# Kernel tuning notes

Measured on AMD Instinct MI355X. Metric: run time of the kernel, lower is better.

## Reference

```python
import jax, jax.numpy as jnp
import numpy as np

D = 512      # feature_bins
DK = 64      # d_k = d_v
H = 8        # n_heads
EPS = 1e-5


def setup_inputs() -> dict:
    key = jax.random.key(0)
    ks = jax.random.split(key, 12)
    B, S = 4, 2048
    s = 1.0 / np.sqrt(D)
    inp = {
        "Q": jax.random.normal(ks[0], (B, S, D), jnp.float32),
        "K": jax.random.normal(ks[1], (B, S, D), jnp.float32),
        "V": jax.random.normal(ks[2], (B, S, D), jnp.float32),
        # nn.Linear params: weight [out, in], bias [out]
        "Wq": jax.random.normal(ks[3], (H * DK, D), jnp.float32) * s,
        "bq": jnp.zeros((H * DK,), jnp.float32),
        "Wk": jax.random.normal(ks[4], (H * DK, D), jnp.float32) * s,
        "bk": jnp.zeros((H * DK,), jnp.float32),
        "Wv": jax.random.normal(ks[5], (H * DK, D), jnp.float32) * s,
        "bv": jnp.zeros((H * DK,), jnp.float32),
        "Wo": jax.random.normal(ks[6], (D, H * DK), jnp.float32) * s,
        "bo": jnp.zeros((D,), jnp.float32),
        "gamma": jnp.ones((D,), jnp.float32),
        "beta": jnp.zeros((D,), jnp.float32),
    }
    return inp


def _layernorm(x, gamma, beta):
    mu = jnp.mean(x, axis=-1, keepdims=True)
    var = jnp.mean(jnp.square(x - mu), axis=-1, keepdims=True)
    return (x - mu) * jax.lax.rsqrt(var + EPS) * gamma + beta


def reference(Q, K, V, Wq, bq, Wk, bk, Wv, bv, Wo, bo, gamma, beta):
    B, S, _ = Q.shape
    residual = Q
    # projections -> [B, H, S, DK]
    q = (Q @ Wq.T + bq).reshape(B, S, H, DK).transpose(0, 2, 1, 3)
    k = (K @ Wk.T + bk).reshape(B, S, H, DK).transpose(0, 2, 1, 3)
    v = (V @ Wv.T + bv).reshape(B, S, H, DK).transpose(0, 2, 1, 3)
    # NOTE: original code has NO 1/sqrt(d_k) scaling
    scores = jnp.einsum("bhqd,bhkd->bhqk", q, k)
    attn = jax.nn.softmax(scores, axis=-1)
    context = jnp.einsum("bhqk,bhkd->bhqd", attn, v)
    context = context.transpose(0, 2, 1, 3).reshape(B, S, H * DK)
    output = context @ Wo.T + bo
    out = _layernorm(output + residual, gamma, beta)
    return (out, attn)
```

## Files before the change

### kernel.cpp

```cpp
#include <hip/hip_runtime.h>

#define NB 4
#define NS 2048
#define ND 512
#define NH 8
#define NDK 64
#define LN_EPS 1e-5f
#define SCLAMP 80.0f

typedef __attribute__((ext_vector_type(8))) short short8;
typedef __attribute__((ext_vector_type(4))) short s16x4;
typedef __attribute__((ext_vector_type(4))) float f32x4;

__device__ inline short f2bf(float x) {
    unsigned u = __builtin_bit_cast(unsigned, x);
    unsigned r = (u + 0x7FFFu + ((u >> 16) & 1u)) >> 16;
    return (short)r;
}
__device__ inline float bf2f(short h) {
    unsigned u = ((unsigned)(unsigned short)h) << 16;
    return __builtin_bit_cast(float, u);
}
__device__ inline unsigned splitT(float x) {
    unsigned u = __builtin_bit_cast(unsigned, x);
    unsigned h = u >> 16;
    float r = x - bf2f((short)h);
    unsigned l = __builtin_bit_cast(unsigned, r) >> 16;
    return (h & 0xFFFFu) | (l << 16);
}

__device__ inline int swzS(int row, int b8) {
    return row * 64 + (((b8) * 8) ^ ((row & 7) << 3));
}
__device__ inline int swz4(int row, int g4) {
    return row * 64 + ((((g4 >> 1)) * 8) ^ ((row & 7) << 3)) + (g4 & 1) * 4;
}

__global__ __launch_bounds__(256) void k_projm_all(
    const float* __restrict__ Qx, const float* __restrict__ Kx,
    const float* __restrict__ Vx,
    const float* __restrict__ Wq, const float* __restrict__ bq,
    const float* __restrict__ Wk, const float* __restrict__ bk,
    const float* __restrict__ Wv, const float* __restrict__ bv,
    short* __restrict__ qh, short* __restrict__ ql,
    short* __restrict__ kh, short* __restrict__ kl,
    short* __restrict__ vtb)
{
    __shared__ short WsH[8192], WsL[8192];
    const int which = blockIdx.z;
    const float* X    = which == 0 ? Qx : (which == 1 ? Kx : Vx);
    const float* W    = which == 0 ? Wq : (which == 1 ? Wk : Wv);
    const float* bias = which == 0 ? bq : (which == 1 ? bk : bv);
    short* outh       = which == 0 ? qh : (which == 1 ? kh : vtb);
    short* outl       = which == 0 ? ql : kl;

    const int tid = threadIdx.x;
    const int w = tid >> 6, lane = tid & 63;
    const int lr = lane & 15, lg = lane >> 4;
    const int row0 = blockIdx.y * 64;
    const int col0 = blockIdx.x * 128;
    const int xrow = row0 + w * 16 + lr;

    f32x4 acc[8] = {};

    float4 wb[8], ab[4];
#pragma unroll
    for (int i = 0; i < 8; ++i) {
        int idx = tid + 256 * i, wrow = idx >> 4, g4 = idx & 15;
        wb[i] = *(const float4*)&W[(size_t)(col0 + wrow) * ND + g4 * 4];
    }
#pragma unroll
    for (int ks = 0; ks < 2; ++ks) {
        ab[2*ks+0] = *(const float4*)&X[(size_t)xrow * ND + ks * 32 + lg * 8];
        ab[2*ks+1] = *(const float4*)&X[(size_t)xrow * ND + ks * 32 + lg * 8 + 4];
    }

    for (int kc = 0; kc < 8; ++kc) {
        __syncthreads();
#pragma unroll
        for (int i = 0; i < 8; ++i) {
            int idx = tid + 256 * i, wrow = idx >> 4, g4 = idx & 15;
            s16x4 hv, lv;
            unsigned p0 = splitT(wb[i].x), p1 = splitT(wb[i].y);
            unsigned p2 = splitT(wb[i].z), p3 = splitT(wb[i].w);
            hv[0] = (short)p0; lv[0] = (short)(p0 >> 16);
            hv[1] = (short)p1; lv[1] = (short)(p1 >> 16);
            hv[2] = (short)p2; lv[2] = (short)(p2 >> 16);
            hv[3] = (short)p3; lv[3] = (short)(p3 >> 16);
            int off = swz4(wrow, g4);
            *(s16x4*)&WsH[off] = hv;
            *(s16x4*)&WsL[off] = lv;
        }
        __syncthreads();

        short8 ah[2], al[2];
#pragma unroll
        for (int ks = 0; ks < 2; ++ks) {
#pragma unroll
            for (int j = 0; j < 4; ++j) {
                unsigned p = splitT(ab[2*ks][j]);
                ah[ks][j] = (short)p; al[ks][j] = (short)(p >> 16);
            }
#pragma unroll
            for (int j = 0; j < 4; ++j) {
                unsigned p = splitT(ab[2*ks+1][j]);
                ah[ks][4+j] = (short)p; al[ks][4+j] = (short)(p >> 16);
            }
        }

        if (kc < 7) {
            const int kn = (kc + 1) * 64;
#pragma unroll
            for (int i = 0; i < 8; ++i) {
                int idx = tid + 256 * i, wrow = idx >> 4, g4 = idx & 15;
                wb[i] = *(const float4*)&W[(size_t)(col0 + wrow) * ND + kn + g4 * 4];
            }
#pragma unroll
            for (int ks = 0; ks < 2; ++ks) {
                ab[2*ks+0] = *(const float4*)&X[(size_t)xrow * ND + kn + ks * 32 + lg * 8];
                ab[2*ks+1] = *(const float4*)&X[(size_t)xrow * ND + kn + ks * 32 + lg * 8 + 4];
            }
        }

#pragma unroll
        for (int cs = 0; cs < 8; ++cs)
#pragma unroll
            for (int ks = 0; ks < 2; ++ks) {
                short8 fh = *(const short8*)&WsH[swzS(cs * 16 + lr, ks * 4 + lg)];
                short8 fl = *(const short8*)&WsL[swzS(cs * 16 + lr, ks * 4 + lg)];
                acc[cs] = __builtin_amdgcn_mfma_f32_16x16x32_bf16(ah[ks], fh, acc[cs], 0, 0, 0);
                acc[cs] = __builtin_amdgcn_mfma_f32_16x16x32_bf16(ah[ks], fl, acc[cs], 0, 0, 0);
                acc[cs] = __builtin_amdgcn_mfma_f32_16x16x32_bf16(al[ks], fh, acc[cs], 0, 0, 0);
            }
    }

#pragma unroll
    for (int cs = 0; cs < 8; ++cs) {
        int c = col0 + cs * 16 + lr;
        int h_ = c >> 6, dk = c & (NDK - 1);
        float bv = bias[c];
#pragma unroll
        for (int r = 0; r < 4; ++r) {
            int gr = row0 + w * 16 + lg * 4 + r;
            int b_ = gr >> 11, s_ = gr & (NS - 1);
            float x = acc[cs][r] + bv;
            if (which != 2) {
                size_t idx = (((size_t)b_ * NH + h_) * NS + s_) * NDK + dk;
                short hb = f2bf(x);
                outh[idx] = hb;
                outl[idx] = f2bf(x - bf2f(hb));
            } else {
                size_t idx = (((size_t)b_ * NH + h_) * NDK + dk) * NS + s_;
                outh[idx] = f2bf(x);
            }
        }
    }
}

__device__ inline void att_decode2(int wg, int& bh, int& rt) {
    rt = (wg >> 3) & 15;
    bh = (wg & 7) + ((wg >> 7) << 3);
}

__global__ __launch_bounds__(256) void k_pvl(
    const short* __restrict__ qh, const short* __restrict__ ql,
    const short* __restrict__ kh, const short* __restrict__ kl,
    const short* __restrict__ vtb,
    float* __restrict__ iLrow, short* __restrict__ ctxb)
{
    __shared__ short KsH[4096], KsL[4096], Vs[4096];
    __shared__ short plbf[4][32][72];
    const int tid = threadIdx.x;
    const int w = tid >> 6, lane = tid & 63;
    const int lr = lane & 15, lg = lane >> 4;
    int bh, rt;
    att_decode2(blockIdx.x, bh, rt);
    const int row0 = rt * 128 + w * 16;
    const size_t base = (size_t)bh * NS * NDK;
    const short* vb = vtb + (size_t)bh * NDK * NS;
    const int srow0 = tid >> 3, sb8 = tid & 7;
    const int srow1 = srow0 + 32;

    short8 ah[2][2], al[2][2];
#pragma unroll
    for (int st = 0; st < 2; ++st)
#pragma unroll
        for (int ks = 0; ks < 2; ++ks) {
            size_t idx = base + (size_t)(row0 + st * 64 + lr) * NDK + ks * 32 + lg * 8;
            ah[st][ks] = *(const short8*)&qh[idx];
            al[st][ks] = *(const short8*)&ql[idx];
        }

    float lsum[2][4] = {};
    f32x4 vacc[2][4] = {};

    short8 nh0, nh1, nl0, nl1, nv0, nv1;
    {
        nh0 = *(const short8*)&kh[base + (size_t)(srow0) * NDK + sb8 * 8];
        nh1 = *(const short8*)&kh[base + (size_t)(srow1) * NDK + sb8 * 8];
        nl0 = *(const short8*)&kl[base + (size_t)(srow0) * NDK + sb8 * 8];
        nl1 = *(const short8*)&kl[base + (size_t)(srow1) * NDK + sb8 * 8];
        nv0 = *(const short8*)&vb[(size_t)srow0 * NS + sb8 * 8];
        nv1 = *(const short8*)&vb[(size_t)srow1 * NS + sb8 * 8];
    }

    for (int c = 0; c < 32; ++c) {
        short8 ch0 = nh0, ch1 = nh1, cl0 = nl0, cl1 = nl1, cv0 = nv0, cv1 = nv1;
        __syncthreads();
        *(short8*)&KsH[swzS(srow0, sb8)] = ch0;
        *(short8*)&KsH[swzS(srow1, sb8)] = ch1;
        *(short8*)&KsL[swzS(srow0, sb8)] = cl0;
        *(short8*)&KsL[swzS(srow1, sb8)] = cl1;
        *(short8*)&Vs[swzS(srow0, sb8)] = cv0;
        *(short8*)&Vs[swzS(srow1, sb8)] = cv1;
        __syncthreads();

        if (c < 31) {
            const int coln = (c + 1) * 64;
            nh0 = *(const short8*)&kh[base + (size_t)(coln + srow0) * NDK + sb8 * 8];
            nh1 = *(const short8*)&kh[base + (size_t)(coln + srow1) * NDK + sb8 * 8];
            nl0 = *(const short8*)&kl[base + (size_t)(coln + srow0) * NDK + sb8 * 8];
            nl1 = *(const short8*)&kl[base + (size_t)(coln + srow1) * NDK + sb8 * 8];
            nv0 = *(const short8*)&vb[(size_t)srow0 * NS + coln + sb8 * 8];
            nv1 = *(const short8*)&vb[(size_t)srow1 * NS + coln + sb8 * 8];
        }

        f32x4 sa[2][4] = {};
#pragma unroll
        for (int cs = 0; cs < 4; ++cs)
#pragma unroll
            for (int ks = 0; ks < 2; ++ks) {
                short8 fh = *(const short8*)&KsH[swzS(cs * 16 + lr, ks * 4 + lg)];
                short8 fl = *(const short8*)&KsL[swzS(cs * 16 + lr, ks * 4 + lg)];
#pragma unroll
                for (int st = 0; st < 2; ++st) {
                    sa[st][cs] = __builtin_amdgcn_mfma_f32_16x16x32_bf16(ah[st][ks], fh, sa[st][cs], 0, 0, 0);
                    sa[st][cs] = __builtin_amdgcn_mfma_f32_16x16x32_bf16(ah[st][ks], fl, sa[st][cs], 0, 0, 0);
                    sa[st][cs] = __builtin_amdgcn_mfma_f32_16x16x32_bf16(al[st][ks], fh, sa[st][cs], 0, 0, 0);
                }
            }

#pragma unroll
        for (int st = 0; st < 2; ++st)
#pragma unroll
            for (int cs = 0; cs < 4; ++cs)
#pragma unroll
                for (int r = 0; r < 4; ++r) {
                    float e = __expf(fminf(sa[st][cs][r], SCLAMP));
                    lsum[st][r] += e;
                    plbf[w][st * 16 + lg * 4 + r][cs * 16 + lr] = f2bf(e);
                }

#pragma unroll
        for (int k2 = 0; k2 < 2; ++k2) {
            short8 pa0 = *(const short8*)&plbf[w][lr][k2 * 32 + lg * 8];
            short8 pa1 = *(const short8*)&plbf[w][16 + lr][k2 * 32 + lg * 8];
#pragma unroll
            for (int d = 0; d < 4; ++d) {
                short8 vf = *(const short8*)&Vs[swzS(d * 16 + lr, k2 * 4 + lg)];
                vacc[0][d] = __builtin_amdgcn_mfma_f32_16x16x32_bf16(pa0, vf, vacc[0][d], 0, 0, 0);
                vacc[1][d] = __builtin_amdgcn_mfma_f32_16x16x32_bf16(pa1, vf, vacc[1][d], 0, 0, 0);
            }
        }
    }

#pragma unroll
    for (int st = 0; st < 2; ++st)
#pragma unroll
        for (int r = 0; r < 4; ++r)
#pragma unroll
            for (int off = 1; off < 16; off <<= 1)
                lsum[st][r] += __shfl_xor(lsum[st][r], off);

    float iL[2][4];
#pragma unroll
    for (int st = 0; st < 2; ++st)
#pragma unroll
        for (int r = 0; r < 4; ++r) iL[st][r] = 1.0f / lsum[st][r];
    if (lr == 0) {
#pragma unroll
        for (int st = 0; st < 2; ++st)
#pragma unroll
            for (int r = 0; r < 4; ++r)
                iLrow[(size_t)bh * NS + row0 + st * 64 + lg * 4 + r] = iL[st][r];
    }
    const int b_ = bh >> 3, h_ = bh & 7;
#pragma unroll
    for (int st = 0; st < 2; ++st)
#pragma unroll
        for (int d = 0; d < 4; ++d)
#pragma unroll
            for (int r = 0; r < 4; ++r) {
                int row = row0 + st * 64 + lg * 4 + r;
                ctxb[((size_t)b_ * NS + row) * ND + h_ * NDK + d * 16 + lr] =
                    f2bf(vacc[st][d][r] * iL[st][r]);
            }
}

__global__ __launch_bounds__(256) void k_attn_write(
    const short* __restrict__ qh, const short* __restrict__ ql,
    const short* __restrict__ kh, const short* __restrict__ kl,
    const float* __restrict__ iLrow, float* __restrict__ attn)
{
    __shared__ short KsH[4096], KsL[4096];
    const int tid = threadIdx.x;
    const int w = tid >> 6, lane = tid & 63;
    const int lr = lane & 15, lg = lane >> 4;
    int bh, rt;
    att_decode2(blockIdx.x, bh, rt);
    const int row0 = rt * 128 + w * 16;
    const size_t base = (size_t)bh * NS * NDK;
    float* ab = attn + (size_t)bh * NS * NS;
    const int srow0 = tid >> 3, sb8 = tid & 7;
    const int srow1 = srow0 + 32;

    short8 ah[2][2], al[2][2];
#pragma unroll
    for (int st = 0; st < 2; ++st)
#pragma unroll
        for (int ks = 0; ks < 2; ++ks) {
            size_t idx = base + (size_t)(row0 + st * 64 + lr) * NDK + ks * 32 + lg * 8;
            ah[st][ks] = *(const short8*)&qh[idx];
            al[st][ks] = *(const short8*)&ql[idx];
        }
    float iLr[2][4];
#pragma unroll
    for (int st = 0; st < 2; ++st)
#pragma unroll
        for (int r = 0; r < 4; ++r)
            iLr[st][r] = iLrow[(size_t)bh * NS + row0 + st * 64 + lg * 4 + r];

    short8 nh0, nh1, nl0, nl1;
    {
        nh0 = *(const short8*)&kh[base + (size_t)(srow0) * NDK + sb8 * 8];
        nh1 = *(const short8*)&kh[base + (size_t)(srow1) * NDK + sb8 * 8];
        nl0 = *(const short8*)&kl[base + (size_t)(srow0) * NDK + sb8 * 8];
        nl1 = *(const short8*)&kl[base + (size_t)(srow1) * NDK + sb8 * 8];
    }

    for (int c = 0; c < 32; ++c) {
        short8 ch0 = nh0, ch1 = nh1, cl0 = nl0, cl1 = nl1;
        __syncthreads();
        *(short8*)&KsH[swzS(srow0, sb8)] = ch0;
        *(short8*)&KsH[swzS(srow1, sb8)] = ch1;
        *(short8*)&KsL[swzS(srow0, sb8)] = cl0;
        *(short8*)&KsL[swzS(srow1, sb8)] = cl1;
        __syncthreads();

        if (c < 31) {
            const int coln = (c + 1) * 64;
            nh0 = *(const short8*)&kh[base + (size_t)(coln + srow0) * NDK + sb8 * 8];
            nh1 = *(const short8*)&kh[base + (size_t)(coln + srow1) * NDK + sb8 * 8];
            nl0 = *(const short8*)&kl[base + (size_t)(coln + srow0) * NDK + sb8 * 8];
            nl1 = *(const short8*)&kl[base + (size_t)(coln + srow1) * NDK + sb8 * 8];
        }

        const int col0 = c * 64;
        f32x4 sa[2][4] = {};
#pragma unroll
        for (int cs = 0; cs < 4; ++cs)
#pragma unroll
            for (int ks = 0; ks < 2; ++ks) {
                short8 fh = *(const short8*)&KsH[swzS(cs * 16 + lr, ks * 4 + lg)];
                short8 fl = *(const short8*)&KsL[swzS(cs * 16 + lr, ks * 4 + lg)];
#pragma unroll
                for (int st = 0; st < 2; ++st) {
                    sa[st][cs] = __builtin_amdgcn_mfma_f32_16x16x32_bf16(ah[st][ks], fh, sa[st][cs], 0, 0, 0);
                    sa[st][cs] = __builtin_amdgcn_mfma_f32_16x16x32_bf16(ah[st][ks], fl, sa[st][cs], 0, 0, 0);
                    sa[st][cs] = __builtin_amdgcn_mfma_f32_16x16x32_bf16(al[st][ks], fh, sa[st][cs], 0, 0, 0);
                }
            }

#pragma unroll
        for (int st = 0; st < 2; ++st)
#pragma unroll
            for (int cs = 0; cs < 4; ++cs)
#pragma unroll
                for (int r = 0; r < 4; ++r) {
                    float p = __expf(fminf(sa[st][cs][r], SCLAMP)) * iLr[st][r];
                    ab[(size_t)(row0 + st * 64 + lg * 4 + r) * NS + col0 + cs * 16 + lr] = p;
                }
    }
}

__global__ __launch_bounds__(256) void k_outproj_m(
    const short* __restrict__ Xc, const float* __restrict__ W,
    const float* __restrict__ bias, const float* __restrict__ Qin,
    float* __restrict__ out)
{
    __shared__ short WsH[8192], WsL[8192];
    const int tid = threadIdx.x;
    const int w = tid >> 6, lane = tid & 63;
    const int lr = lane & 15, lg = lane >> 4;
    const int row0 = blockIdx.y * 64;
    const int col0 = blockIdx.x * 128;
    const int xrow = row0 + w * 16 + lr;

    f32x4 acc[8] = {};

    float4 wb[8];
    short8 abn[2];
#pragma unroll
    for (int i = 0; i < 8; ++i) {
        int idx = tid + 256 * i, wrow = idx >> 4, g4 = idx & 15;
        wb[i] = *(const float4*)&W[(size_t)(col0 + wrow) * ND + g4 * 4];
    }
#pragma unroll
    for (int ks = 0; ks < 2; ++ks)
        abn[ks] = *(const short8*)&Xc[(size_t)xrow * ND + ks * 32 + lg * 8];

    for (int kc = 0; kc < 8; ++kc) {
        __syncthreads();
#pragma unroll
        for (int i = 0; i < 8; ++i) {
            int idx = tid + 256 * i, wrow = idx >> 4, g4 = idx & 15;
            s16x4 hv, lv;
            unsigned p0 = splitT(wb[i].x), p1 = splitT(wb[i].y);
            unsigned p2 = splitT(wb[i].z), p3 = splitT(wb[i].w);
            hv[0] = (short)p0; lv[0] = (short)(p0 >> 16);
            hv[1] = (short)p1; lv[1] = (short)(p1 >> 16);
            hv[2] = (short)p2; lv[2] = (short)(p2 >> 16);
            hv[3] = (short)p3; lv[3] = (short)(p3 >> 16);
            int off = swz4(wrow, g4);
            *(s16x4*)&WsH[off] = hv;
            *(s16x4*)&WsL[off] = lv;
        }
        __syncthreads();

        short8 ah[2] = { abn[0], abn[1] };

        if (kc < 7) {
            const int kn = (kc + 1) * 64;
#pragma unroll
            for (int i = 0; i < 8; ++i) {
                int idx = tid + 256 * i, wrow = idx >> 4, g4 = idx & 15;
                wb[i] = *(const float4*)&W[(size_t)(col0 + wrow) * ND + kn + g4 * 4];
            }
#pragma unroll
            for (int ks = 0; ks < 2; ++ks)
                abn[ks] = *(const short8*)&Xc[(size_t)xrow * ND + kn + ks * 32 + lg * 8];
        }

#pragma unroll
        for (int cs = 0; cs < 8; ++cs)
#pragma unroll
            for (int ks = 0; ks < 2; ++ks) {
                short8 fh = *(const short8*)&WsH[swzS(cs * 16 + lr, ks * 4 + lg)];
                short8 fl = *(const short8*)&WsL[swzS(cs * 16 + lr, ks * 4 + lg)];
                acc[cs] = __builtin_amdgcn_mfma_f32_16x16x32_bf16(ah[ks], fh, acc[cs], 0, 0, 0);
                acc[cs] = __builtin_amdgcn_mfma_f32_16x16x32_bf16(ah[ks], fl, acc[cs], 0, 0, 0);
            }
    }

#pragma unroll
    for (int cs = 0; cs < 8; ++cs) {
        int c = col0 + cs * 16 + lr;
        float bv = bias[c];
#pragma unroll
        for (int r = 0; r < 4; ++r) {
            int gr = row0 + w * 16 + lg * 4 + r;
            float res = Qin[(size_t)gr * ND + c];
            out[(size_t)gr * ND + c] = acc[cs][r] + bv + res;
        }
    }
}

__global__ __launch_bounds__(256) void k_ln(
    float* __restrict__ out, const float* __restrict__ gamma,
    const float* __restrict__ beta)
{
    const int tid = threadIdx.x;
    float* p = out + (size_t)blockIdx.x * ND;
    float2 v = *(const float2*)&p[tid * 2];

    float s = v.x + v.y;
#pragma unroll
    for (int off = 32; off > 0; off >>= 1) s += __shfl_xor(s, off);
    __shared__ float red1[4];
    __shared__ float red2[4];
    if ((tid & 63) == 0) red1[tid >> 6] = s;
    __syncthreads();
    const float mu = (red1[0] + red1[1] + red1[2] + red1[3]) * (1.0f / ND);

    float dx = v.x - mu, dy = v.y - mu;
    float q = dx * dx + dy * dy;
#pragma unroll
    for (int off = 32; off > 0; off >>= 1) q += __shfl_xor(q, off);
    if ((tid & 63) == 0) red2[tid >> 6] = q;
    __syncthreads();
    const float var = (red2[0] + red2[1] + red2[2] + red2[3]) * (1.0f / ND);
    const float inv = rsqrtf(var + LN_EPS);

    float2 g = *(const float2*)&gamma[tid * 2];
    float2 be = *(const float2*)&beta[tid * 2];
    float2 o = { dx * inv * g.x + be.x, dy * inv * g.y + be.y };
    *(float2*)&p[tid * 2] = o;
}

extern "C" void kernel_launch(void* const* d_in, const int* in_sizes, int n_in,
                              void* d_out, int out_size, void* d_ws, size_t ws_size,
                              hipStream_t stream)
{
    const float* Q    = (const float*)d_in[0];
    const float* K    = (const float*)d_in[1];
    const float* V    = (const float*)d_in[2];
    const float* Wq   = (const float*)d_in[3];
    const float* bq   = (const float*)d_in[4];
    const float* Wk   = (const float*)d_in[5];
    const float* bk   = (const float*)d_in[6];
    const float* Wv   = (const float*)d_in[7];
    const float* bv   = (const float*)d_in[8];
    const float* Wo   = (const float*)d_in[9];
    const float* bo   = (const float*)d_in[10];
    const float* gam  = (const float*)d_in[11];
    const float* bet  = (const float*)d_in[12];

    float* out  = (float*)d_out;
    float* attn = out + (size_t)NB * NS * ND;

    const size_t QKV = (size_t)NB * NH * NS * NDK;
    short* qh   = (short*)d_ws;
    short* ql   = qh + QKV;
    short* kh   = ql + QKV;
    short* kl   = kh + QKV;
    short* vtb  = kl + QKV;
    short* ctxb = vtb + QKV;
    float* iLrow = (float*)(ctxb + QKV);

    dim3 blk(256);

    dim3 gP(ND / 128, (NB * NS) / 64, 3);
    k_projm_all<<<gP, blk, 0, stream>>>(Q, K, V, Wq, bq, Wk, bk, Wv, bv,
                                        qh, ql, kh, kl, vtb);

    dim3 gAtt((NS / 128) * NB * NH);
    k_pvl<<<gAtt, blk, 0, stream>>>(qh, ql, kh, kl, vtb, iLrow, ctxb);
    k_attn_write<<<gAtt, blk, 0, stream>>>(qh, ql, kh, kl, iLrow, attn);

    dim3 gO(ND / 128, (NB * NS) / 64);
    k_outproj_m<<<gO, blk, 0, stream>>>(ctxb, Wo, bo, Q, out);

    k_ln<<<dim3(NB * NS), blk, 0, stream>>>(out, gam, bet);
}
```

Baseline: 331.0 us.

## Fuse attention-prob write into PV kernel and switch softmax to exp2

Merges the two attention kernels into one: after the first pass computes row sums and the context, the same workgroup runs a second pass over K to recompute scores and write the normalized probabilities. The inverse row sums stay in registers, so the iLrow round-trip, the Q reload and one kernel launch go away. Q is pre-scaled by log2(e) in the projection so the kernel can use the hardware exp2 instead of __expf, and the clamp is raised to match the new scale. Register pressure and code size of the fused kernel go up.

```diff
diff --git a/kernel.cpp b/kernel.cpp
--- a/kernel.cpp
+++ b/kernel.cpp
@@ -6,7 +6,8 @@
 #define NH 8
 #define NDK 64
 #define LN_EPS 1e-5f
-#define SCLAMP 80.0f
+#define SCLAMP 115.0f
+#define LOG2E 1.44269504f
 
 typedef __attribute__((ext_vector_type(8))) short short8;
 typedef __attribute__((ext_vector_type(4))) short s16x4;
@@ -144,6 +145,7 @@
             int gr = row0 + w * 16 + lg * 4 + r;
             int b_ = gr >> 11, s_ = gr & (NS - 1);
             float x = acc[cs][r] + bv;
+            if (which == 0) x *= LOG2E;
             if (which != 2) {
                 size_t idx = (((size_t)b_ * NH + h_) * NS + s_) * NDK + dk;
                 short hb = f2bf(x);
@@ -162,11 +164,11 @@
     bh = (wg & 7) + ((wg >> 7) << 3);
 }
 
-__global__ __launch_bounds__(256) void k_pvl(
+__global__ __launch_bounds__(256) void k_att(
     const short* __restrict__ qh, const short* __restrict__ ql,
     const short* __restrict__ kh, const short* __restrict__ kl,
     const short* __restrict__ vtb,
-    float* __restrict__ iLrow, short* __restrict__ ctxb)
+    short* __restrict__ ctxb, float* __restrict__ attn)
 {
     __shared__ short KsH[4096], KsL[4096], Vs[4096];
     __shared__ short plbf[4][32][72];
@@ -178,6 +180,7 @@
     const int row0 = rt * 128 + w * 16;
     const size_t base = (size_t)bh * NS * NDK;
     const short* vb = vtb + (size_t)bh * NDK * NS;
+    float* ab = attn + (size_t)bh * NS * NS;
     const int srow0 = tid >> 3, sb8 = tid & 7;
     const int srow1 = srow0 + 32;
 
@@ -246,7 +249,7 @@
             for (int cs = 0; cs < 4; ++cs)
 #pragma unroll
                 for (int r = 0; r < 4; ++r) {
-                    float e = __expf(fminf(sa[st][cs][r], SCLAMP));
+                    float e = __builtin_amdgcn_exp2f(fminf(sa[st][cs][r], SCLAMP));
                     lsum[st][r] += e;
                     plbf[w][st * 16 + lg * 4 + r][cs * 16 + lr] = f2bf(e);
                 }
@@ -277,13 +280,7 @@
     for (int st = 0; st < 2; ++st)
 #pragma unroll
         for (int r = 0; r < 4; ++r) iL[st][r] = 1.0f / lsum[st][r];
-    if (lr == 0) {
-#pragma unroll
-        for (int st = 0; st < 2; ++st)
-#pragma unroll
-            for (int r = 0; r < 4; ++r)
-                iLrow[(size_t)bh * NS + row0 + st * 64 + lg * 4 + r] = iL[st][r];
-    }
+
     const int b_ = bh >> 3, h_ = bh & 7;
 #pragma unroll
     for (int st = 0; st < 2; ++st)
@@ -295,42 +292,7 @@
                 ctxb[((size_t)b_ * NS + row) * ND + h_ * NDK + d * 16 + lr] =
                     f2bf(vacc[st][d][r] * iL[st][r]);
             }
-}
-
-__global__ __launch_bounds__(256) void k_attn_write(
-    const short* __restrict__ qh, const short* __restrict__ ql,
-    const short* __restrict__ kh, const short* __restrict__ kl,
-    const float* __restrict__ iLrow, float* __restrict__ attn)
-{
-    __shared__ short KsH[4096], KsL[4096];
-    const int tid = threadIdx.x;
-    const int w = tid >> 6, lane = tid & 63;
-    const int lr = lane & 15, lg = lane >> 4;
-    int bh, rt;
-    att_decode2(blockIdx.x, bh, rt);
-    const int row0 = rt * 128 + w * 16;
-    const size_t base = (size_t)bh * NS * NDK;
-    float* ab = attn + (size_t)bh * NS * NS;
-    const int srow0 = tid >> 3, sb8 = tid & 7;
-    const int srow1 = srow0 + 32;
-
-    short8 ah[2][2], al[2][2];
-#pragma unroll
-    for (int st = 0; st < 2; ++st)
-#pragma unroll
-        for (int ks = 0; ks < 2; ++ks) {
-            size_t idx = base + (size_t)(row0 + st * 64 + lr) * NDK + ks * 32 + lg * 8;
-            ah[st][ks] = *(const short8*)&qh[idx];
-            al[st][ks] = *(const short8*)&ql[idx];
-        }
-    float iLr[2][4];
-#pragma unroll
-    for (int st = 0; st < 2; ++st)
-#pragma unroll
-        for (int r = 0; r < 4; ++r)
-            iLr[st][r] = iLrow[(size_t)bh * NS + row0 + st * 64 + lg * 4 + r];
-
-    short8 nh0, nh1, nl0, nl1;
+
     {
         nh0 = *(const short8*)&kh[base + (size_t)(srow0) * NDK + sb8 * 8];
         nh1 = *(const short8*)&kh[base + (size_t)(srow1) * NDK + sb8 * 8];
@@ -377,7 +339,7 @@
             for (int cs = 0; cs < 4; ++cs)
 #pragma unroll
                 for (int r = 0; r < 4; ++r) {
-                    float p = __expf(fminf(sa[st][cs][r], SCLAMP)) * iLr[st][r];
+                    float p = __builtin_amdgcn_exp2f(fminf(sa[st][cs][r], SCLAMP)) * iL[st][r];
                     ab[(size_t)(row0 + st * 64 + lg * 4 + r) * NS + col0 + cs * 16 + lr] = p;
                 }
     }
@@ -525,7 +487,6 @@
     short* kl   = kh + QKV;
     short* vtb  = kl + QKV;
     short* ctxb = vtb + QKV;
-    float* iLrow = (float*)(ctxb + QKV);
 
     dim3 blk(256);
 
@@ -534,8 +495,7 @@
                                         qh, ql, kh, kl, vtb);
 
     dim3 gAtt((NS / 128) * NB * NH);
-    k_pvl<<<gAtt, blk, 0, stream>>>(qh, ql, kh, kl, vtb, iLrow, ctxb);
-    k_attn_write<<<gAtt, blk, 0, stream>>>(qh, ql, kh, kl, iLrow, attn);
+    k_att<<<gAtt, blk, 0, stream>>>(qh, ql, kh, kl, vtb, ctxb, attn);
 
     dim3 gO(ND / 128, (NB * NS) / 64);
     k_outproj_m<<<gO, blk, 0, stream>>>(ctxb, Wo, bo, Q, out);
```

Result: faster. 307.2 us (median of 2 runs) (-7.2%).
